# Kernel tuning notes

Hardware: AMD Instinct MI355X
Metric: run time of the kernel (lower is better)

## Reference

```python
import jax, jax.numpy as jnp
import numpy as np

N, E, CLIP, HID, H, P, MD, B = 4096, 16384, 512, 1024, 4, 4, 512, 32
OUT2 = P * MD  # 2048


def prelu(x, a):
    return jnp.where(x >= 0, x, a * x)


def add_self_loops(src, dst, edge_attr, n):
    # PyG fill_value='mean': self-loop edge_attr = mean of incoming edge attrs
    sums = jax.ops.segment_sum(edge_attr, dst, num_segments=n)
    cnt = jax.ops.segment_sum(jnp.ones((dst.shape[0], 1), edge_attr.dtype), dst, num_segments=n)
    loop_attr = sums / jnp.maximum(cnt, 1.0)
    idx = jnp.arange(n)
    return (jnp.concatenate([src, idx]), jnp.concatenate([dst, idx]),
            jnp.concatenate([edge_attr, loop_attr], axis=0))


def gat_conv(x, src, dst, edge_attr, W, asrc, adst, We, ae, bias, heads, c):
    # PyG GATConv, concat=False (mean over heads), edge_dim used only in attention
    n = x.shape[0]
    src, dst, edge_attr = add_self_loops(src, dst, edge_attr, n)
    h = (x @ W).reshape(n, heads, c)                      # [N,H,C]
    e = (edge_attr @ We).reshape(-1, heads, c)            # [E',H,C]
    a_s = jnp.einsum('nhc,hc->nh', h, asrc)
    a_d = jnp.einsum('nhc,hc->nh', h, adst)
    a_e = jnp.einsum('ehc,hc->eh', e, ae)
    alpha = jax.nn.leaky_relu(a_s[src] + a_d[dst] + a_e, 0.2)  # [E',H]
    amax = jax.ops.segment_max(alpha, dst, num_segments=n)
    ex = jnp.exp(alpha - amax[dst])
    denom = jax.ops.segment_sum(ex, dst, num_segments=n)
    w = ex / jnp.maximum(denom[dst], 1e-16)
    msg = h[src] * w[:, :, None]                          # [E',H,C]
    out = jax.ops.segment_sum(msg, dst, num_segments=n)   # [N,H,C]
    return out.mean(axis=1) + bias


def attentional_pool(x, batch, gW1, gb1, gp1, gW2, gb2, gp2, gW3, gb3, n_graphs):
    gate = prelu(x @ gW1 + gb1, gp1)
    gate = prelu(gate @ gW2 + gb2, gp2)
    gate = gate @ gW3 + gb3                               # [N,1]
    gmax = jax.ops.segment_max(gate, batch, num_segments=n_graphs)
    ex = jnp.exp(gate - gmax[batch])
    denom = jax.ops.segment_sum(ex, batch, num_segments=n_graphs)
    s = ex / jnp.maximum(denom[batch], 1e-16)             # [N,1]
    return jax.ops.segment_sum(s * x, batch, num_segments=n_graphs)  # [B,F]


def setup_inputs() -> dict:
    key = jax.random.key(0)
    ks = jax.random.split(key, 24)
    sc = 0.05
    inp = {
        'x': jax.random.normal(ks[0], (N, CLIP), jnp.float32),
        'edge_index': jax.random.randint(ks[1], (2, E), 0, N),
        'edge_attr': jax.random.normal(ks[2], (E, CLIP), jnp.float32),
        'batch': jnp.sort(jax.random.randint(ks[3], (N,), 0, B)),
        # GATConv 1
        'W1': jax.random.normal(ks[4], (CLIP, H * HID), jnp.float32) * sc,
        'asrc1': jax.random.normal(ks[5], (H, HID), jnp.float32) * sc,
        'adst1': jax.random.normal(ks[6], (H, HID), jnp.float32) * sc,
        'We1': jax.random.normal(ks[7], (CLIP, H * HID), jnp.float32) * sc,
        'ae1': jax.random.normal(ks[8], (H, HID), jnp.float32) * sc,
        'b1': jnp.zeros((HID,), jnp.float32),
        'p1': jnp.float32(0.25),
        # GATConv 2
        'W2': jax.random.normal(ks[9], (HID, H * OUT2), jnp.float32) * sc,
        'asrc2': jax.random.normal(ks[10], (H, OUT2), jnp.float32) * sc,
        'adst2': jax.random.normal(ks[11], (H, OUT2), jnp.float32) * sc,
        'We2': jax.random.normal(ks[12], (CLIP, H * OUT2), jnp.float32) * sc,
        'ae2': jax.random.normal(ks[13], (H, OUT2), jnp.float32) * sc,
        'b2': jnp.zeros((OUT2,), jnp.float32),
        'p2': jnp.float32(0.25),
        # AttentionalAggregation gate_nn
        'gW1': jax.random.normal(ks[14], (OUT2, HID), jnp.float32) * sc,
        'gb1': jnp.zeros((HID,), jnp.float32),
        'gp1': jnp.float32(0.25),
        'gW2': jax.random.normal(ks[15], (HID, HID), jnp.float32) * sc,
        'gb2': jnp.zeros((HID,), jnp.float32),
        'gp2': jnp.float32(0.25),
        'gW3': jax.random.normal(ks[16], (HID, 1), jnp.float32) * sc,
        'gb3': jnp.zeros((1,), jnp.float32),
    }
    return inp


def reference(x, edge_index, edge_attr, batch,
              W1, asrc1, adst1, We1, ae1, b1, p1,
              W2, asrc2, adst2, We2, ae2, b2, p2,
              gW1, gb1, gp1, gW2, gb2, gp2, gW3, gb3):
    src, dst = edge_index[0], edge_index[1]
    h = gat_conv(x, src, dst, edge_attr, W1, asrc1, adst1, We1, ae1, b1, H, HID)
    h = prelu(h, p1)
    h = gat_conv(h, src, dst, edge_attr, W2, asrc2, adst2, We2, ae2, b2, H, OUT2)
    h = prelu(h, p2)
    pooled = attentional_pool(h, batch, gW1, gb1, gp1, gW2, gb2, gp2, gW3, gb3, B)
    return pooled.reshape(-1, P, MD)  # [B, prefix_length, mbart_dim]
```

## Files before the change

### kernel.cpp

```cpp
#include <hip/hip_runtime.h>
#include <hip/hip_bf16.h>
#include <math.h>

#define N_NODES 4096
#define N_EDGES 16384
#define CLIPD   512
#define HID     1024
#define NH      4
#define OUTD    2048
#define NB      32

typedef __bf16 bf16_t;
typedef bf16_t bf16x8 __attribute__((ext_vector_type(8)));
typedef float f32x4 __attribute__((ext_vector_type(4)));

static __device__ __forceinline__ float lrelu(float x) { return x >= 0.f ? x : 0.2f * x; }

static __device__ __forceinline__ unsigned short f2bf(float f) {
  union { float f; unsigned int u; } v; v.f = f;
  unsigned int u = v.u;
  unsigned int r = (u + 0x7FFFu + ((u >> 16) & 1u)) >> 16;
  return (unsigned short)r;
}
static __device__ __forceinline__ float bf2f(unsigned short u) {
  union { unsigned int i; float f; } v; v.i = ((unsigned int)u) << 16; return v.f;
}

#define GLDS(g, l) __builtin_amdgcn_global_load_lds( \
    (const __attribute__((address_space(1))) void*)(g), \
    (__attribute__((address_space(3))) void*)(l), 16, 0, 0)

__global__ __launch_bounds__(256) void cvt_kernel(const float* __restrict__ in,
                                                  unsigned short* __restrict__ out, int n4) {
  int i = blockIdx.x * 256 + threadIdx.x;
  if (i < n4) {
    float4 f = ((const float4*)in)[i];
    ushort4 o;
    o.x = f2bf(f.x); o.y = f2bf(f.y); o.z = f2bf(f.z); o.w = f2bf(f.w);
    ((ushort4*)out)[i] = o;
  }
}

__global__ __launch_bounds__(256) void tcvt_kernel(const float* __restrict__ in,
                                                   unsigned short* __restrict__ out,
                                                   int K, int N) {
  __shared__ float t[32][33];
  const int k0 = blockIdx.y * 32, n0 = blockIdx.x * 32;
  const int tx = threadIdx.x, ty = threadIdx.y;
#pragma unroll
  for (int i = 0; i < 4; ++i) t[ty + 8 * i][tx] = in[(size_t)(k0 + ty + 8 * i) * N + n0 + tx];
  __syncthreads();
#pragma unroll
  for (int i = 0; i < 4; ++i) out[(size_t)(n0 + ty + 8 * i) * K + k0 + tx] = f2bf(t[tx][ty + 8 * i]);
}

template<int C>
__global__ __launch_bounds__(256) void v_kernel(const float* __restrict__ We,
                                                const float* __restrict__ ae,
                                                float* __restrict__ v) {
  const int k = blockIdx.x;
  const int tid = threadIdx.x;
  const float* row = We + (size_t)k * (NH * C);
  float acc[NH] = {0.f, 0.f, 0.f, 0.f};
  for (int c = tid; c < C; c += 256) {
    for (int h = 0; h < NH; ++h) acc[h] += row[h * C + c] * ae[h * C + c];
  }
  for (int h = 0; h < NH; ++h)
    for (int o = 32; o > 0; o >>= 1) acc[h] += __shfl_down(acc[h], o);
  __shared__ float red[4][NH];
  const int wid = tid >> 6, lane = tid & 63;
  if (lane == 0)
    for (int h = 0; h < NH; ++h) red[wid][h] = acc[h];
  __syncthreads();
  if (tid < NH) v[k * NH + tid] = red[0][tid] + red[1][tid] + red[2][tid] + red[3][tid];
}

__global__ void deg_kernel(const int* __restrict__ ei, int* __restrict__ deg) {
  int e = blockIdx.x * 256 + threadIdx.x;
  if (e < N_EDGES) atomicAdd(&deg[ei[N_EDGES + e]], 1);
}

__global__ __launch_bounds__(1024) void scan_kernel(const int* __restrict__ deg, int* __restrict__ offs) {
  __shared__ int s[1024];
  const int t = threadIdx.x;
  int d0 = deg[4 * t], d1 = deg[4 * t + 1], d2 = deg[4 * t + 2], d3 = deg[4 * t + 3];
  s[t] = d0 + d1 + d2 + d3;
  __syncthreads();
  for (int off = 1; off < 1024; off <<= 1) {
    int v = (t >= off) ? s[t - off] : 0;
    __syncthreads();
    s[t] += v;
    __syncthreads();
  }
  int base = (t > 0) ? s[t - 1] : 0;
  offs[4 * t] = base;
  offs[4 * t + 1] = base + d0;
  offs[4 * t + 2] = base + d0 + d1;
  offs[4 * t + 3] = base + d0 + d1 + d2;
  if (t == 1023) offs[4096] = s[1023];
}

__global__ void fill_kernel(const int* __restrict__ ei, const int* __restrict__ offs,
                            int* __restrict__ cursor, int* __restrict__ csr_src,
                            int* __restrict__ csr_eid) {
  int e = blockIdx.x * 256 + threadIdx.x;
  if (e >= N_EDGES) return;
  int dst = ei[N_EDGES + e];
  int pos = offs[dst] + atomicAdd(&cursor[dst], 1);
  csr_src[pos] = ei[e];
  csr_eid[pos] = e;
}

__global__ __launch_bounds__(256) void ae_kernel(const float* __restrict__ ea, const int* __restrict__ ei,
                                                 const float* __restrict__ v1, const float* __restrict__ v2,
                                                 float* __restrict__ ae1, float* __restrict__ ae2,
                                                 float* __restrict__ aesum1, float* __restrict__ aesum2) {
  __shared__ float4 v1s[CLIPD];
  __shared__ float4 v2s[CLIPD];
  const int tid = threadIdx.x;
  v1s[tid] = ((const float4*)v1)[tid];
  v1s[tid + 256] = ((const float4*)v1)[tid + 256];
  v2s[tid] = ((const float4*)v2)[tid];
  v2s[tid + 256] = ((const float4*)v2)[tid + 256];
  __syncthreads();
  const int wid = tid >> 6, lane = tid & 63;
  for (int i = 0; i < 16; ++i) {
    const int e = blockIdx.x * 64 + wid * 16 + i;
    const float* row = ea + (size_t)e * CLIPD;
    float a1[NH] = {0.f, 0.f, 0.f, 0.f}, a2[NH] = {0.f, 0.f, 0.f, 0.f};
    for (int k = lane; k < CLIPD; k += 64) {
      float x = row[k];
      float4 w1 = v1s[k];
      float4 w2 = v2s[k];
      a1[0] += x * w1.x; a1[1] += x * w1.y; a1[2] += x * w1.z; a1[3] += x * w1.w;
      a2[0] += x * w2.x; a2[1] += x * w2.y; a2[2] += x * w2.z; a2[3] += x * w2.w;
    }
    for (int h = 0; h < NH; ++h)
      for (int o = 32; o > 0; o >>= 1) {
        a1[h] += __shfl_down(a1[h], o);
        a2[h] += __shfl_down(a2[h], o);
      }
    if (lane == 0) {
      int dst = ei[N_EDGES + e];
      for (int h = 0; h < NH; ++h) {
        ae1[e * NH + h] = a1[h];
        ae2[e * NH + h] = a2[h];
        atomicAdd(&aesum1[dst * NH + h], a1[h]);
        atomicAdd(&aesum2[dst * NH + h], a2[h]);
      }
    }
  }
}

__global__ void loopdiv_kernel(float* __restrict__ s1, float* __restrict__ s2,
                               const int* __restrict__ deg) {
  int i = blockIdx.x * 256 + threadIdx.x;
  if (i >= N_NODES * NH) return;
  float c = fmaxf((float)deg[i >> 2], 1.0f);
  s1[i] /= c;
  s2[i] /= c;
}

template<int EPI>
__global__ __launch_bounds__(256) void mfma_gemm(const unsigned short* __restrict__ A,
                                                 const unsigned short* __restrict__ Bt,
                                                 unsigned short* __restrict__ C,
                                                 int M, int N, int K,
                                                 const float* __restrict__ bias,
                                                 const float* __restrict__ pa) {
  __shared__ unsigned short As[128 * 32];
  __shared__ unsigned short Bs[128 * 32];
  const int tid = threadIdx.x;
  const int lane = tid & 63;
  const int w = tid >> 6;
  const int wr = w >> 1, wc = w & 1;
  const int brow = blockIdx.y * 128, bcol = blockIdx.x * 128;
  const int r0 = tid >> 2;
  const int koff = (tid & 3) * 8;
  const int fr = lane & 15;
  const int fk = (lane >> 4) * 8;
  f32x4 acc[4][4] = {};
  for (int kt = 0; kt < K; kt += 32) {
    GLDS(A + (size_t)(brow + r0) * K + kt + koff, &As[tid * 8]);
    GLDS(A + (size_t)(brow + 64 + r0) * K + kt + koff, &As[2048 + tid * 8]);
    GLDS(Bt + (size_t)(bcol + r0) * K + kt + koff, &Bs[tid * 8]);
    GLDS(Bt + (size_t)(bcol + 64 + r0) * K + kt + koff, &Bs[2048 + tid * 8]);
    asm volatile("s_waitcnt vmcnt(0)" ::: "memory");
    __syncthreads();
    bf16x8 af[4], bfr[4];
#pragma unroll
    for (int mi = 0; mi < 4; ++mi)
      af[mi] = *(const bf16x8*)&As[(wr * 64 + mi * 16 + fr) * 32 + fk];
#pragma unroll
    for (int ni = 0; ni < 4; ++ni)
      bfr[ni] = *(const bf16x8*)&Bs[(wc * 64 + ni * 16 + fr) * 32 + fk];
#pragma unroll
    for (int mi = 0; mi < 4; ++mi)
#pragma unroll
      for (int ni = 0; ni < 4; ++ni)
        acc[mi][ni] = __builtin_amdgcn_mfma_f32_16x16x32_bf16(af[mi], bfr[ni], acc[mi][ni], 0, 0, 0);
    __syncthreads();
  }
  const float ap = EPI ? *pa : 0.f;
#pragma unroll
  for (int mi = 0; mi < 4; ++mi) {
    const int rb = brow + wr * 64 + mi * 16 + (lane >> 4) * 4;
#pragma unroll
    for (int ni = 0; ni < 4; ++ni) {
      const int col = bcol + wc * 64 + ni * 16 + fr;
      float bv = 0.f;
      if (EPI) bv = bias[col];
#pragma unroll
      for (int r = 0; r < 4; ++r) {
        float v = acc[mi][ni][r];
        if (EPI) { v += bv; v = v >= 0.f ? v : ap * v; }
        C[(size_t)(rb + r) * N + col] = f2bf(v);
      }
    }
  }
}

template<int C>
__global__ __launch_bounds__(256) void nodedot_kernel(const unsigned short* __restrict__ hbuf,
                                                      const float* __restrict__ asrc,
                                                      const float* __restrict__ adst,
                                                      float* __restrict__ as_, float* __restrict__ ad_) {
  const int n = blockIdx.x, tid = threadIdx.x;
  const unsigned short* row = hbuf + (size_t)n * (NH * C);
  float s[NH] = {0.f, 0.f, 0.f, 0.f}, d[NH] = {0.f, 0.f, 0.f, 0.f};
  for (int c4 = tid; c4 < C / 4; c4 += 256) {
#pragma unroll
    for (int h = 0; h < NH; ++h) {
      ushort4 u = *(const ushort4*)&row[h * C + c4 * 4];
      float4 av = *(const float4*)&asrc[h * C + c4 * 4];
      float4 dv = *(const float4*)&adst[h * C + c4 * 4];
      float f0 = bf2f(u.x), f1 = bf2f(u.y), f2 = bf2f(u.z), f3 = bf2f(u.w);
      s[h] += f0 * av.x + f1 * av.y + f2 * av.z + f3 * av.w;
      d[h] += f0 * dv.x + f1 * dv.y + f2 * dv.z + f3 * dv.w;
    }
  }
  for (int h = 0; h < NH; ++h)
    for (int o = 32; o > 0; o >>= 1) {
      s[h] += __shfl_down(s[h], o);
      d[h] += __shfl_down(d[h], o);
    }
  __shared__ float rs[4][NH], rd[4][NH];
  const int wid = tid >> 6, lane = tid & 63;
  if (lane == 0)
    for (int h = 0; h < NH; ++h) {
      rs[wid][h] = s[h];
      rd[wid][h] = d[h];
    }
  __syncthreads();
  if (tid < NH)
    as_[n * NH + tid] = rs[0][tid] + rs[1][tid] + rs[2][tid] + rs[3][tid];
  else if (tid < 2 * NH) {
    int h = tid - NH;
    ad_[n * NH + h] = rd[0][h] + rd[1][h] + rd[2][h] + rd[3][h];
  }
}

template<int C, int OUTMODE>
__global__ __launch_bounds__(256) void agg_kernel(const unsigned short* __restrict__ hbuf,
                                                  const float* __restrict__ as_, const float* __restrict__ ad_,
                                                  const float* __restrict__ aee, const float* __restrict__ aeloop,
                                                  const int* __restrict__ offs, const int* __restrict__ csr_src,
                                                  const int* __restrict__ csr_eid,
                                                  const float* __restrict__ bias, const float* __restrict__ pa,
                                                  float* __restrict__ outf, unsigned short* __restrict__ outb) {
  constexpr int HC = NH * C;
  constexpr int C4 = C / 1024;
  const int n = blockIdx.x;
  const int tid = threadIdx.x;
  const int off = offs[n];
  const int deg = offs[n + 1] - off;
  __shared__ float minv[NH], dinv[NH], wself[NH];
  __shared__ float wch[32][NH];
  __shared__ int sch[32];
  if (tid < 64) {
    const int h = tid >> 4, slot = tid & 15;
    const float adn = ad_[n * NH + h];
    const float aself = lrelu(as_[n * NH + h] + adn + aeloop[n * NH + h]);
    float m = (slot == 0) ? aself : -3.0e38f;
    for (int i = slot; i < deg; i += 16) {
      float a = lrelu(as_[csr_src[off + i] * NH + h] + adn + aee[csr_eid[off + i] * NH + h]);
      m = fmaxf(m, a);
    }
    for (int o = 1; o < 16; o <<= 1) m = fmaxf(m, __shfl_xor(m, o));
    float den = (slot == 0) ? __expf(aself - m) : 0.f;
    for (int i = slot; i < deg; i += 16) {
      float a = lrelu(as_[csr_src[off + i] * NH + h] + adn + aee[csr_eid[off + i] * NH + h]);
      den += __expf(a - m);
    }
    for (int o = 1; o < 16; o <<= 1) den += __shfl_xor(den, o);
    if (slot == 0) {
      minv[h] = m;
      dinv[h] = 1.0f / den;
      wself[h] = __expf(aself - m) / den;
    }
  }
  __syncthreads();
  float acc[NH][C4 * 4];
#pragma unroll
  for (int h = 0; h < NH; ++h)
#pragma unroll
    for (int c = 0; c < C4 * 4; ++c) acc[h][c] = 0.f;
  for (int base = 0; base < deg; base += 32) {
    const int cnt = min(32, deg - base);
    if (tid < cnt * NH) {
      const int i = tid >> 2, h = tid & 3;
      const int sidx = csr_src[off + base + i];
      float a = lrelu(as_[sidx * NH + h] + ad_[n * NH + h] + aee[csr_eid[off + base + i] * NH + h]);
      wch[i][h] = __expf(a - minv[h]) * dinv[h];
      if (h == 0) sch[i] = sidx;
    }
    __syncthreads();
    for (int i = 0; i < cnt; ++i) {
      const unsigned short* hp = hbuf + (size_t)sch[i] * HC;
#pragma unroll
      for (int h = 0; h < NH; ++h) {
        const float wv = wch[i][h];
#pragma unroll
        for (int c = 0; c < C4; ++c) {
          ushort4 u = *(const ushort4*)&hp[h * C + (c * 256 + tid) * 4];
          acc[h][c * 4 + 0] += wv * bf2f(u.x);
          acc[h][c * 4 + 1] += wv * bf2f(u.y);
          acc[h][c * 4 + 2] += wv * bf2f(u.z);
          acc[h][c * 4 + 3] += wv * bf2f(u.w);
        }
      }
    }
    __syncthreads();
  }
  {
    const unsigned short* hp = hbuf + (size_t)n * HC;
#pragma unroll
    for (int h = 0; h < NH; ++h) {
      const float wv = wself[h];
#pragma unroll
      for (int c = 0; c < C4; ++c) {
        ushort4 u = *(const ushort4*)&hp[h * C + (c * 256 + tid) * 4];
        acc[h][c * 4 + 0] += wv * bf2f(u.x);
        acc[h][c * 4 + 1] += wv * bf2f(u.y);
        acc[h][c * 4 + 2] += wv * bf2f(u.z);
        acc[h][c * 4 + 3] += wv * bf2f(u.w);
      }
    }
  }
  const float ap = *pa;
#pragma unroll
  for (int c = 0; c < C4; ++c) {
    const int cb = (c * 256 + tid) * 4;
    float4 vf;
    ushort4 vb;
    float* vp = &vf.x;
#pragma unroll
    for (int j = 0; j < 4; ++j) {
      float v = 0.25f * (acc[0][c * 4 + j] + acc[1][c * 4 + j] + acc[2][c * 4 + j] + acc[3][c * 4 + j])
                + bias[cb + j];
      v = v >= 0.f ? v : ap * v;
      vp[j] = v;
    }
    vb.x = f2bf(vf.x); vb.y = f2bf(vf.y); vb.z = f2bf(vf.z); vb.w = f2bf(vf.w);
    if (OUTMODE == 1) *(float4*)&outf[(size_t)n * C + cb] = vf;
    *(ushort4*)&outb[(size_t)n * C + cb] = vb;
  }
}

__global__ __launch_bounds__(256) void gate3_kernel(const unsigned short* __restrict__ gh2,
                                                    const float* __restrict__ gW3,
                                                    const float* __restrict__ gb3, float* __restrict__ gate) {
  const int n = blockIdx.x, tid = threadIdx.x;
  const unsigned short* row = gh2 + (size_t)n * HID;
  ushort4 u = *(const ushort4*)&row[tid * 4];
  float4 wv = *(const float4*)&gW3[tid * 4];
  float acc = bf2f(u.x) * wv.x + bf2f(u.y) * wv.y + bf2f(u.z) * wv.z + bf2f(u.w) * wv.w;
  for (int o = 32; o > 0; o >>= 1) acc += __shfl_down(acc, o);
  __shared__ float red[4];
  const int wid = tid >> 6, lane = tid & 63;
  if (lane == 0) red[wid] = acc;
  __syncthreads();
  if (tid == 0) gate[n] = red[0] + red[1] + red[2] + red[3] + gb3[0];
}

__global__ void gstart_kernel(const int* __restrict__ batch, int* __restrict__ gstart) {
  int n = blockIdx.x * 256 + threadIdx.x;
  if (n >= N_NODES) return;
  int b = batch[n];
  if (n == 0) {
    for (int bb = 0; bb <= b; ++bb) gstart[bb] = 0;
  } else {
    int pb = batch[n - 1];
    for (int bb = pb + 1; bb <= b; ++bb) gstart[bb] = n;
  }
  if (n == N_NODES - 1)
    for (int bb = b + 1; bb <= NB; ++bb) gstart[bb] = N_NODES;
}

__global__ __launch_bounds__(256) void gsoft_kernel(const float* __restrict__ gate, const int* __restrict__ gstart,
                                                    float* __restrict__ gm, float* __restrict__ ginv) {
  const int b = blockIdx.x, tid = threadIdx.x;
  const int s = gstart[b], e = gstart[b + 1];
  float m = -3.0e38f;
  for (int n = s + tid; n < e; n += 256) m = fmaxf(m, gate[n]);
  for (int o = 32; o > 0; o >>= 1) m = fmaxf(m, __shfl_down(m, o));
  __shared__ float red[4];
  __shared__ float red2[4];
  const int wid = tid >> 6, lane = tid & 63;
  if (lane == 0) red[wid] = m;
  __syncthreads();
  m = fmaxf(fmaxf(red[0], red[1]), fmaxf(red[2], red[3]));
  float sum = 0.f;
  for (int n = s + tid; n < e; n += 256) sum += __expf(gate[n] - m);
  for (int o = 32; o > 0; o >>= 1) sum += __shfl_down(sum, o);
  if (lane == 0) red2[wid] = sum;
  __syncthreads();
  if (tid == 0) {
    sum = red2[0] + red2[1] + red2[2] + red2[3];
    gm[b] = m;
    ginv[b] = 1.0f / fmaxf(sum, 1e-16f);
  }
}

__global__ __launch_bounds__(256) void pool_kernel(const float* __restrict__ out2, const float* __restrict__ gate,
                                                   const float* __restrict__ gm, const float* __restrict__ ginv,
                                                   const int* __restrict__ gstart, float* __restrict__ dout) {
  const int b = blockIdx.y;
  const int col = blockIdx.x * 256 + threadIdx.x;
  const int s = gstart[b], e = gstart[b + 1];
  const float m = gm[b], gi = ginv[b];
  float acc = 0.f;
  for (int n = s; n < e; ++n) {
    float w = __expf(gate[n] - m) * gi;
    acc += w * out2[(size_t)n * OUTD + col];
  }
  dout[(size_t)b * OUTD + col] = acc;
}

#define MB(x) ((size_t)(x) * 1048576)
#define WS_XB     MB(0)
#define WS_W1T    MB(4)
#define WS_H1B    MB(8)
#define WS_H2B    MB(0)
#define WS_OUT1B  MB(64)
#define WS_W2T    MB(72)
#define WS_OUT2F  MB(88)
#define WS_OUT2B  MB(120)
#define WS_GH1B   MB(136)
#define WS_GH2B   MB(144)
#define WS_GW1T   MB(152)
#define WS_GW2T   MB(156)
#define WS_SM     MB(158)
#define WS_DEG    (WS_SM + 0)
#define WS_CUR    (WS_SM + 16384)
#define WS_AES1   (WS_SM + 32768)
#define WS_AES2   (WS_SM + 98304)
#define WS_ZBYTES 163840
#define WS_OFFS   (WS_SM + 163840)
#define WS_CSRS   (WS_OFFS + 16640)
#define WS_CSRE   (WS_CSRS + 65536)
#define WS_AS1    (WS_CSRE + 65536)
#define WS_AD1    (WS_AS1 + 65536)
#define WS_AEE1   (WS_AD1 + 65536)
#define WS_AS2    (WS_AEE1 + 262144)
#define WS_AD2    (WS_AS2 + 65536)
#define WS_AEE2   (WS_AD2 + 65536)
#define WS_V1     (WS_AEE2 + 262144)
#define WS_V2     (WS_V1 + 8192)
#define WS_GATE   (WS_V2 + 8192)
#define WS_GM     (WS_GATE + 16384)
#define WS_GINV   (WS_GM + 128)
#define WS_GSTART (WS_GINV + 128)

extern "C" void kernel_launch(void* const* d_in, const int* in_sizes, int n_in,
                              void* d_out, int out_size, void* d_ws, size_t ws_size,
                              hipStream_t stream) {
  const float* x     = (const float*)d_in[0];
  const int*   ei    = (const int*)d_in[1];
  const float* ea    = (const float*)d_in[2];
  const int*   batch = (const int*)d_in[3];
  const float* W1    = (const float*)d_in[4];
  const float* asrc1 = (const float*)d_in[5];
  const float* adst1 = (const float*)d_in[6];
  const float* We1   = (const float*)d_in[7];
  const float* ae1w  = (const float*)d_in[8];
  const float* b1    = (const float*)d_in[9];
  const float* p1    = (const float*)d_in[10];
  const float* W2    = (const float*)d_in[11];
  const float* asrc2 = (const float*)d_in[12];
  const float* adst2 = (const float*)d_in[13];
  const float* We2   = (const float*)d_in[14];
  const float* ae2w  = (const float*)d_in[15];
  const float* b2    = (const float*)d_in[16];
  const float* p2    = (const float*)d_in[17];
  const float* gW1   = (const float*)d_in[18];
  const float* gb1   = (const float*)d_in[19];
  const float* gp1   = (const float*)d_in[20];
  const float* gW2   = (const float*)d_in[21];
  const float* gb2   = (const float*)d_in[22];
  const float* gp2   = (const float*)d_in[23];
  const float* gW3   = (const float*)d_in[24];
  const float* gb3   = (const float*)d_in[25];

  char* ws = (char*)d_ws;
  unsigned short* xb    = (unsigned short*)(ws + WS_XB);
  unsigned short* W1t   = (unsigned short*)(ws + WS_W1T);
  unsigned short* h1b   = (unsigned short*)(ws + WS_H1B);
  unsigned short* h2b   = (unsigned short*)(ws + WS_H2B);
  unsigned short* out1b = (unsigned short*)(ws + WS_OUT1B);
  unsigned short* W2t   = (unsigned short*)(ws + WS_W2T);
  float*          out2f = (float*)(ws + WS_OUT2F);
  unsigned short* out2b = (unsigned short*)(ws + WS_OUT2B);
  unsigned short* gh1b  = (unsigned short*)(ws + WS_GH1B);
  unsigned short* gh2b  = (unsigned short*)(ws + WS_GH2B);
  unsigned short* gW1t  = (unsigned short*)(ws + WS_GW1T);
  unsigned short* gW2t  = (unsigned short*)(ws + WS_GW2T);
  int*   deg     = (int*)(ws + WS_DEG);
  int*   cursor  = (int*)(ws + WS_CUR);
  float* aesum1  = (float*)(ws + WS_AES1);
  float* aesum2  = (float*)(ws + WS_AES2);
  int*   offs    = (int*)(ws + WS_OFFS);
  int*   csr_src = (int*)(ws + WS_CSRS);
  int*   csr_eid = (int*)(ws + WS_CSRE);
  float* as1     = (float*)(ws + WS_AS1);
  float* ad1     = (float*)(ws + WS_AD1);
  float* aee1    = (float*)(ws + WS_AEE1);
  float* as2     = (float*)(ws + WS_AS2);
  float* ad2     = (float*)(ws + WS_AD2);
  float* aee2    = (float*)(ws + WS_AEE2);
  float* v1      = (float*)(ws + WS_V1);
  float* v2      = (float*)(ws + WS_V2);
  float* gate    = (float*)(ws + WS_GATE);
  float* gm      = (float*)(ws + WS_GM);
  float* ginv    = (float*)(ws + WS_GINV);
  int*   gstart  = (int*)(ws + WS_GSTART);
  float* dout    = (float*)d_out;

  hipMemsetAsync(ws + WS_DEG, 0, WS_ZBYTES, stream);

  cvt_kernel<<<(N_NODES * CLIPD / 4 + 255) / 256, 256, 0, stream>>>(x, xb, N_NODES * CLIPD / 4);
  tcvt_kernel<<<dim3(4096 / 32, 512 / 32), dim3(32, 8), 0, stream>>>(W1, W1t, CLIPD, NH * HID);
  tcvt_kernel<<<dim3(8192 / 32, 1024 / 32), dim3(32, 8), 0, stream>>>(W2, W2t, HID, NH * OUTD);
  tcvt_kernel<<<dim3(1024 / 32, 2048 / 32), dim3(32, 8), 0, stream>>>(gW1, gW1t, OUTD, HID);
  tcvt_kernel<<<dim3(1024 / 32, 1024 / 32), dim3(32, 8), 0, stream>>>(gW2, gW2t, HID, HID);

  v_kernel<HID><<<CLIPD, 256, 0, stream>>>(We1, ae1w, v1);
  v_kernel<OUTD><<<CLIPD, 256, 0, stream>>>(We2, ae2w, v2);

  deg_kernel<<<N_EDGES / 256, 256, 0, stream>>>(ei, deg);
  scan_kernel<<<1, 1024, 0, stream>>>(deg, offs);
  fill_kernel<<<N_EDGES / 256, 256, 0, stream>>>(ei, offs, cursor, csr_src, csr_eid);

  mfma_gemm<0><<<dim3(32, 32), 256, 0, stream>>>(xb, W1t, h1b, N_NODES, NH * HID, CLIPD, nullptr, nullptr);

  ae_kernel<<<N_EDGES / 64, 256, 0, stream>>>(ea, ei, v1, v2, aee1, aee2, aesum1, aesum2);
  loopdiv_kernel<<<(N_NODES * NH) / 256, 256, 0, stream>>>(aesum1, aesum2, deg);

  nodedot_kernel<HID><<<N_NODES, 256, 0, stream>>>(h1b, asrc1, adst1, as1, ad1);
  agg_kernel<HID, 0><<<N_NODES, 256, 0, stream>>>(h1b, as1, ad1, aee1, aesum1, offs, csr_src, csr_eid,
                                                  b1, p1, nullptr, out1b);

  mfma_gemm<0><<<dim3(64, 32), 256, 0, stream>>>(out1b, W2t, h2b, N_NODES, NH * OUTD, HID, nullptr, nullptr);

  nodedot_kernel<OUTD><<<N_NODES, 256, 0, stream>>>(h2b, asrc2, adst2, as2, ad2);
  agg_kernel<OUTD, 1><<<N_NODES, 256, 0, stream>>>(h2b, as2, ad2, aee2, aesum2, offs, csr_src, csr_eid,
                                                   b2, p2, out2f, out2b);

  mfma_gemm<1><<<dim3(8, 32), 256, 0, stream>>>(out2b, gW1t, gh1b, N_NODES, HID, OUTD, gb1, gp1);
  mfma_gemm<1><<<dim3(8, 32), 256, 0, stream>>>(gh1b, gW2t, gh2b, N_NODES, HID, HID, gb2, gp2);
  gate3_kernel<<<N_NODES, 256, 0, stream>>>(gh2b, gW3, gb3, gate);

  gstart_kernel<<<N_NODES / 256, 256, 0, stream>>>(batch, gstart);
  gsoft_kernel<<<NB, 256, 0, stream>>>(gate, gstart, gm, ginv);
  pool_kernel<<<dim3(OUTD / 256, NB), 256, 0, stream>>>(out2f, gate, gm, ginv, gstart, dout);
}
```

Before: 585.9 us.

## Aggregate before projecting in GAT layers and fold attention vectors into weights

Each GAT layer now aggregates per-head attention-weighted input features (x or out1) first. It then does a single GEMM against per-head stacked transposed weights, scaled by 0.25 so the head mean folds into K, with the bias and PReLU applied in the GEMM epilogue. The attention logits a_s and a_d are computed directly from the input rows using precomputed W·asrc and W·adst vectors, which removes the need to materialize the wide h = xW tensor. This shrinks the gather traffic from NH*C-wide rows to input-width rows and removes the large [N, H*C] intermediates. In exchange the GEMM K dimension grows by NH, and attention is now computed on fp32 x or bf16 out1 rather than on the bf16 projected features.

```diff
diff --git a/kernel.cpp b/kernel.cpp
--- a/kernel.cpp
+++ b/kernel.cpp
@@ -54,16 +54,33 @@
   for (int i = 0; i < 4; ++i) out[(size_t)(n0 + ty + 8 * i) * K + k0 + tx] = f2bf(t[tx][ty + 8 * i]);
 }
 
+template<int K1, int N1>
+__global__ __launch_bounds__(256) void stack_tcvt_kernel(const float* __restrict__ in,
+                                                         unsigned short* __restrict__ out,
+                                                         float scale) {
+  __shared__ float t[32][33];
+  const int h = blockIdx.z;
+  const int k0 = blockIdx.y * 32, n0 = blockIdx.x * 32;
+  const int tx = threadIdx.x, ty = threadIdx.y;
+#pragma unroll
+  for (int i = 0; i < 4; ++i)
+    t[ty + 8 * i][tx] = in[(size_t)(k0 + ty + 8 * i) * (NH * N1) + h * N1 + n0 + tx];
+  __syncthreads();
+#pragma unroll
+  for (int i = 0; i < 4; ++i)
+    out[(size_t)(n0 + ty + 8 * i) * (NH * K1) + h * K1 + k0 + tx] = f2bf(scale * t[tx][ty + 8 * i]);
+}
+
 template<int C>
-__global__ __launch_bounds__(256) void v_kernel(const float* __restrict__ We,
-                                                const float* __restrict__ ae,
+__global__ __launch_bounds__(256) void v_kernel(const float* __restrict__ W,
+                                                const float* __restrict__ a,
                                                 float* __restrict__ v) {
   const int k = blockIdx.x;
   const int tid = threadIdx.x;
-  const float* row = We + (size_t)k * (NH * C);
+  const float* row = W + (size_t)k * (NH * C);
   float acc[NH] = {0.f, 0.f, 0.f, 0.f};
   for (int c = tid; c < C; c += 256) {
-    for (int h = 0; h < NH; ++h) acc[h] += row[h * C + c] * ae[h * C + c];
+    for (int h = 0; h < NH; ++h) acc[h] += row[h * C + c] * a[h * C + c];
   }
   for (int h = 0; h < NH; ++h)
     for (int o = 32; o > 0; o >>= 1) acc[h] += __shfl_down(acc[h], o);
@@ -73,6 +90,39 @@
     for (int h = 0; h < NH; ++h) red[wid][h] = acc[h];
   __syncthreads();
   if (tid < NH) v[k * NH + tid] = red[0][tid] + red[1][tid] + red[2][tid] + red[3][tid];
+}
+
+template<int C>
+__global__ __launch_bounds__(256) void v2_kernel(const float* __restrict__ W,
+                                                 const float* __restrict__ a1v,
+                                                 const float* __restrict__ a2v,
+                                                 float* __restrict__ o1, float* __restrict__ o2) {
+  const int k = blockIdx.x;
+  const int tid = threadIdx.x;
+  const float* row = W + (size_t)k * (NH * C);
+  float x1[NH] = {0.f, 0.f, 0.f, 0.f}, x2[NH] = {0.f, 0.f, 0.f, 0.f};
+  for (int c = tid; c < C; c += 256) {
+    for (int h = 0; h < NH; ++h) {
+      float w = row[h * C + c];
+      x1[h] += w * a1v[h * C + c];
+      x2[h] += w * a2v[h * C + c];
+    }
+  }
+  for (int h = 0; h < NH; ++h)
+    for (int o = 32; o > 0; o >>= 1) {
+      x1[h] += __shfl_down(x1[h], o);
+      x2[h] += __shfl_down(x2[h], o);
+    }
+  __shared__ float r1[4][NH], r2[4][NH];
+  const int wid = tid >> 6, lane = tid & 63;
+  if (lane == 0)
+    for (int h = 0; h < NH; ++h) { r1[wid][h] = x1[h]; r2[wid][h] = x2[h]; }
+  __syncthreads();
+  if (tid < NH) o1[k * NH + tid] = r1[0][tid] + r1[1][tid] + r1[2][tid] + r1[3][tid];
+  else if (tid < 2 * NH) {
+    int h = tid - NH;
+    o2[k * NH + h] = r2[0][h] + r2[1][h] + r2[2][h] + r2[3][h];
+  }
 }
 
 __global__ void deg_kernel(const int* __restrict__ ei, int* __restrict__ deg) {
@@ -161,10 +211,184 @@
   s2[i] /= c;
 }
 
-template<int EPI>
+__global__ __launch_bounds__(256) void rowdot_x(const float* __restrict__ x,
+                                                const float* __restrict__ us, const float* __restrict__ ud,
+                                                float* __restrict__ as_, float* __restrict__ ad_) {
+  __shared__ float4 su[CLIPD], sd[CLIPD];
+  const int tid = threadIdx.x;
+  for (int k = tid; k < CLIPD; k += 256) {
+    su[k] = ((const float4*)us)[k];
+    sd[k] = ((const float4*)ud)[k];
+  }
+  __syncthreads();
+  const int wid = tid >> 6, lane = tid & 63;
+  const int n = blockIdx.x * 4 + wid;
+  const float* row = x + (size_t)n * CLIPD;
+  float s[NH] = {0.f, 0.f, 0.f, 0.f}, d[NH] = {0.f, 0.f, 0.f, 0.f};
+  for (int k = lane; k < CLIPD; k += 64) {
+    float xv = row[k];
+    float4 u = su[k], v = sd[k];
+    s[0] += xv * u.x; s[1] += xv * u.y; s[2] += xv * u.z; s[3] += xv * u.w;
+    d[0] += xv * v.x; d[1] += xv * v.y; d[2] += xv * v.z; d[3] += xv * v.w;
+  }
+#pragma unroll
+  for (int h = 0; h < NH; ++h)
+    for (int o = 32; o > 0; o >>= 1) {
+      s[h] += __shfl_down(s[h], o);
+      d[h] += __shfl_down(d[h], o);
+    }
+  if (lane == 0)
+    for (int h = 0; h < NH; ++h) {
+      as_[n * NH + h] = s[h];
+      ad_[n * NH + h] = d[h];
+    }
+}
+
+__global__ __launch_bounds__(256) void rowdot_o(const unsigned short* __restrict__ rows,
+                                                const float* __restrict__ us, const float* __restrict__ ud,
+                                                float* __restrict__ as_, float* __restrict__ ad_) {
+  __shared__ float4 su[HID], sd[HID];
+  const int tid = threadIdx.x;
+  for (int k = tid; k < HID; k += 256) {
+    su[k] = ((const float4*)us)[k];
+    sd[k] = ((const float4*)ud)[k];
+  }
+  __syncthreads();
+  const int wid = tid >> 6, lane = tid & 63;
+  const int n = blockIdx.x * 4 + wid;
+  const unsigned short* row = rows + (size_t)n * HID;
+  float s[NH] = {0.f, 0.f, 0.f, 0.f}, d[NH] = {0.f, 0.f, 0.f, 0.f};
+  for (int k2 = lane; k2 < HID / 2; k2 += 64) {
+    ushort2 uv = ((const ushort2*)row)[k2];
+    float f0 = bf2f(uv.x), f1 = bf2f(uv.y);
+    float4 u0 = su[2 * k2], u1 = su[2 * k2 + 1];
+    float4 v0 = sd[2 * k2], v1 = sd[2 * k2 + 1];
+    s[0] += f0 * u0.x + f1 * u1.x; s[1] += f0 * u0.y + f1 * u1.y;
+    s[2] += f0 * u0.z + f1 * u1.z; s[3] += f0 * u0.w + f1 * u1.w;
+    d[0] += f0 * v0.x + f1 * v1.x; d[1] += f0 * v0.y + f1 * v1.y;
+    d[2] += f0 * v0.z + f1 * v1.z; d[3] += f0 * v0.w + f1 * v1.w;
+  }
+#pragma unroll
+  for (int h = 0; h < NH; ++h)
+    for (int o = 32; o > 0; o >>= 1) {
+      s[h] += __shfl_down(s[h], o);
+      d[h] += __shfl_down(d[h], o);
+    }
+  if (lane == 0)
+    for (int h = 0; h < NH; ++h) {
+      as_[n * NH + h] = s[h];
+      ad_[n * NH + h] = d[h];
+    }
+}
+
+template<int C>
+__global__ __launch_bounds__(256) void aggn_kernel(const unsigned short* __restrict__ src,
+                                                   const float* __restrict__ as_, const float* __restrict__ ad_,
+                                                   const float* __restrict__ aee, const float* __restrict__ aeloop,
+                                                   const int* __restrict__ offs, const int* __restrict__ csr_src,
+                                                   const int* __restrict__ csr_eid,
+                                                   unsigned short* __restrict__ out) {
+  constexpr int CPT = C / 256;
+  const int n = blockIdx.x;
+  const int tid = threadIdx.x;
+  const int off = offs[n];
+  const int deg = offs[n + 1] - off;
+  __shared__ float minv[NH], dinv[NH], wself[NH];
+  __shared__ float wch[32][NH];
+  __shared__ int sch[32];
+  if (tid < 64) {
+    const int h = tid >> 4, slot = tid & 15;
+    const float adn = ad_[n * NH + h];
+    const float aself = lrelu(as_[n * NH + h] + adn + aeloop[n * NH + h]);
+    float m = (slot == 0) ? aself : -3.0e38f;
+    for (int i = slot; i < deg; i += 16) {
+      float a = lrelu(as_[csr_src[off + i] * NH + h] + adn + aee[csr_eid[off + i] * NH + h]);
+      m = fmaxf(m, a);
+    }
+    for (int o = 1; o < 16; o <<= 1) m = fmaxf(m, __shfl_xor(m, o));
+    float den = (slot == 0) ? __expf(aself - m) : 0.f;
+    for (int i = slot; i < deg; i += 16) {
+      float a = lrelu(as_[csr_src[off + i] * NH + h] + adn + aee[csr_eid[off + i] * NH + h]);
+      den += __expf(a - m);
+    }
+    for (int o = 1; o < 16; o <<= 1) den += __shfl_xor(den, o);
+    if (slot == 0) {
+      minv[h] = m;
+      dinv[h] = 1.0f / den;
+      wself[h] = __expf(aself - m) / den;
+    }
+  }
+  __syncthreads();
+  float acc[NH][CPT];
+#pragma unroll
+  for (int h = 0; h < NH; ++h)
+#pragma unroll
+    for (int c = 0; c < CPT; ++c) acc[h][c] = 0.f;
+  for (int base = 0; base < deg; base += 32) {
+    const int cnt = min(32, deg - base);
+    if (tid < cnt * NH) {
+      const int i = tid >> 2, h = tid & 3;
+      const int sidx = csr_src[off + base + i];
+      float a = lrelu(as_[sidx * NH + h] + ad_[n * NH + h] + aee[csr_eid[off + base + i] * NH + h]);
+      wch[i][h] = __expf(a - minv[h]) * dinv[h];
+      if (h == 0) sch[i] = sidx;
+    }
+    __syncthreads();
+    for (int i = 0; i < cnt; ++i) {
+      const unsigned short* hp = src + (size_t)sch[i] * C + tid * CPT;
+      float f[CPT];
+      if constexpr (CPT == 2) {
+        ushort2 u = *(const ushort2*)hp;
+        f[0] = bf2f(u.x); f[1] = bf2f(u.y);
+      } else {
+        ushort4 u = *(const ushort4*)hp;
+        f[0] = bf2f(u.x); f[1] = bf2f(u.y); f[2] = bf2f(u.z); f[3] = bf2f(u.w);
+      }
+#pragma unroll
+      for (int h = 0; h < NH; ++h) {
+        const float wv = wch[i][h];
+#pragma unroll
+        for (int c = 0; c < CPT; ++c) acc[h][c] += wv * f[c];
+      }
+    }
+    __syncthreads();
+  }
+  {
+    const unsigned short* hp = src + (size_t)n * C + tid * CPT;
+    float f[CPT];
+    if constexpr (CPT == 2) {
+      ushort2 u = *(const ushort2*)hp;
+      f[0] = bf2f(u.x); f[1] = bf2f(u.y);
+    } else {
+      ushort4 u = *(const ushort4*)hp;
+      f[0] = bf2f(u.x); f[1] = bf2f(u.y); f[2] = bf2f(u.z); f[3] = bf2f(u.w);
+    }
+#pragma unroll
+    for (int h = 0; h < NH; ++h) {
+      const float wv = wself[h];
+#pragma unroll
+      for (int c = 0; c < CPT; ++c) acc[h][c] += wv * f[c];
+    }
+  }
+#pragma unroll
+  for (int h = 0; h < NH; ++h) {
+    if constexpr (CPT == 2) {
+      ushort2 o;
+      o.x = f2bf(acc[h][0]); o.y = f2bf(acc[h][1]);
+      *(ushort2*)&out[((size_t)n * NH + h) * C + tid * 2] = o;
+    } else {
+      ushort4 o;
+      o.x = f2bf(acc[h][0]); o.y = f2bf(acc[h][1]); o.z = f2bf(acc[h][2]); o.w = f2bf(acc[h][3]);
+      *(ushort4*)&out[((size_t)n * NH + h) * C + tid * 4] = o;
+    }
+  }
+}
+
+template<int EPI, int WF>
 __global__ __launch_bounds__(256) void mfma_gemm(const unsigned short* __restrict__ A,
                                                  const unsigned short* __restrict__ Bt,
                                                  unsigned short* __restrict__ C,
+                                                 float* __restrict__ Cf,
                                                  int M, int N, int K,
                                                  const float* __restrict__ bias,
                                                  const float* __restrict__ pa) {
@@ -215,155 +439,9 @@
         float v = acc[mi][ni][r];
         if (EPI) { v += bv; v = v >= 0.f ? v : ap * v; }
         C[(size_t)(rb + r) * N + col] = f2bf(v);
+        if (WF) Cf[(size_t)(rb + r) * N + col] = v;
       }
     }
-  }
-}
-
-template<int C>
-__global__ __launch_bounds__(256) void nodedot_kernel(const unsigned short* __restrict__ hbuf,
-                                                      const float* __restrict__ asrc,
-                                                      const float* __restrict__ adst,
-                                                      float* __restrict__ as_, float* __restrict__ ad_) {
-  const int n = blockIdx.x, tid = threadIdx.x;
-  const unsigned short* row = hbuf + (size_t)n * (NH * C);
-  float s[NH] = {0.f, 0.f, 0.f, 0.f}, d[NH] = {0.f, 0.f, 0.f, 0.f};
-  for (int c4 = tid; c4 < C / 4; c4 += 256) {
-#pragma unroll
-    for (int h = 0; h < NH; ++h) {
-      ushort4 u = *(const ushort4*)&row[h * C + c4 * 4];
-      float4 av = *(const float4*)&asrc[h * C + c4 * 4];
-      float4 dv = *(const float4*)&adst[h * C + c4 * 4];
-      float f0 = bf2f(u.x), f1 = bf2f(u.y), f2 = bf2f(u.z), f3 = bf2f(u.w);
-      s[h] += f0 * av.x + f1 * av.y + f2 * av.z + f3 * av.w;
-      d[h] += f0 * dv.x + f1 * dv.y + f2 * dv.z + f3 * dv.w;
-    }
-  }
-  for (int h = 0; h < NH; ++h)
-    for (int o = 32; o > 0; o >>= 1) {
-      s[h] += __shfl_down(s[h], o);
-      d[h] += __shfl_down(d[h], o);
-    }
-  __shared__ float rs[4][NH], rd[4][NH];
-  const int wid = tid >> 6, lane = tid & 63;
-  if (lane == 0)
-    for (int h = 0; h < NH; ++h) {
-      rs[wid][h] = s[h];
-      rd[wid][h] = d[h];
-    }
-  __syncthreads();
-  if (tid < NH)
-    as_[n * NH + tid] = rs[0][tid] + rs[1][tid] + rs[2][tid] + rs[3][tid];
-  else if (tid < 2 * NH) {
-    int h = tid - NH;
-    ad_[n * NH + h] = rd[0][h] + rd[1][h] + rd[2][h] + rd[3][h];
-  }
-}
-
-template<int C, int OUTMODE>
-__global__ __launch_bounds__(256) void agg_kernel(const unsigned short* __restrict__ hbuf,
-                                                  const float* __restrict__ as_, const float* __restrict__ ad_,
-                                                  const float* __restrict__ aee, const float* __restrict__ aeloop,
-                                                  const int* __restrict__ offs, const int* __restrict__ csr_src,
-                                                  const int* __restrict__ csr_eid,
-                                                  const float* __restrict__ bias, const float* __restrict__ pa,
-                                                  float* __restrict__ outf, unsigned short* __restrict__ outb) {
-  constexpr int HC = NH * C;
-  constexpr int C4 = C / 1024;
-  const int n = blockIdx.x;
-  const int tid = threadIdx.x;
-  const int off = offs[n];
-  const int deg = offs[n + 1] - off;
-  __shared__ float minv[NH], dinv[NH], wself[NH];
-  __shared__ float wch[32][NH];
-  __shared__ int sch[32];
-  if (tid < 64) {
-    const int h = tid >> 4, slot = tid & 15;
-    const float adn = ad_[n * NH + h];
-    const float aself = lrelu(as_[n * NH + h] + adn + aeloop[n * NH + h]);
-    float m = (slot == 0) ? aself : -3.0e38f;
-    for (int i = slot; i < deg; i += 16) {
-      float a = lrelu(as_[csr_src[off + i] * NH + h] + adn + aee[csr_eid[off + i] * NH + h]);
-      m = fmaxf(m, a);
-    }
-    for (int o = 1; o < 16; o <<= 1) m = fmaxf(m, __shfl_xor(m, o));
-    float den = (slot == 0) ? __expf(aself - m) : 0.f;
-    for (int i = slot; i < deg; i += 16) {
-      float a = lrelu(as_[csr_src[off + i] * NH + h] + adn + aee[csr_eid[off + i] * NH + h]);
-      den += __expf(a - m);
-    }
-    for (int o = 1; o < 16; o <<= 1) den += __shfl_xor(den, o);
-    if (slot == 0) {
-      minv[h] = m;
-      dinv[h] = 1.0f / den;
-      wself[h] = __expf(aself - m) / den;
-    }
-  }
-  __syncthreads();
-  float acc[NH][C4 * 4];
-#pragma unroll
-  for (int h = 0; h < NH; ++h)
-#pragma unroll
-    for (int c = 0; c < C4 * 4; ++c) acc[h][c] = 0.f;
-  for (int base = 0; base < deg; base += 32) {
-    const int cnt = min(32, deg - base);
-    if (tid < cnt * NH) {
-      const int i = tid >> 2, h = tid & 3;
-      const int sidx = csr_src[off + base + i];
-      float a = lrelu(as_[sidx * NH + h] + ad_[n * NH + h] + aee[csr_eid[off + base + i] * NH + h]);
-      wch[i][h] = __expf(a - minv[h]) * dinv[h];
-      if (h == 0) sch[i] = sidx;
-    }
-    __syncthreads();
-    for (int i = 0; i < cnt; ++i) {
-      const unsigned short* hp = hbuf + (size_t)sch[i] * HC;
-#pragma unroll
-      for (int h = 0; h < NH; ++h) {
-        const float wv = wch[i][h];
-#pragma unroll
-        for (int c = 0; c < C4; ++c) {
-          ushort4 u = *(const ushort4*)&hp[h * C + (c * 256 + tid) * 4];
-          acc[h][c * 4 + 0] += wv * bf2f(u.x);
-          acc[h][c * 4 + 1] += wv * bf2f(u.y);
-          acc[h][c * 4 + 2] += wv * bf2f(u.z);
-          acc[h][c * 4 + 3] += wv * bf2f(u.w);
-        }
-      }
-    }
-    __syncthreads();
-  }
-  {
-    const unsigned short* hp = hbuf + (size_t)n * HC;
-#pragma unroll
-    for (int h = 0; h < NH; ++h) {
-      const float wv = wself[h];
-#pragma unroll
-      for (int c = 0; c < C4; ++c) {
-        ushort4 u = *(const ushort4*)&hp[h * C + (c * 256 + tid) * 4];
-        acc[h][c * 4 + 0] += wv * bf2f(u.x);
-        acc[h][c * 4 + 1] += wv * bf2f(u.y);
-        acc[h][c * 4 + 2] += wv * bf2f(u.z);
-        acc[h][c * 4 + 3] += wv * bf2f(u.w);
-      }
-    }
-  }
-  const float ap = *pa;
-#pragma unroll
-  for (int c = 0; c < C4; ++c) {
-    const int cb = (c * 256 + tid) * 4;
-    float4 vf;
-    ushort4 vb;
-    float* vp = &vf.x;
-#pragma unroll
-    for (int j = 0; j < 4; ++j) {
-      float v = 0.25f * (acc[0][c * 4 + j] + acc[1][c * 4 + j] + acc[2][c * 4 + j] + acc[3][c * 4 + j])
-                + bias[cb + j];
-      v = v >= 0.f ? v : ap * v;
-      vp[j] = v;
-    }
-    vb.x = f2bf(vf.x); vb.y = f2bf(vf.y); vb.z = f2bf(vf.z); vb.w = f2bf(vf.w);
-    if (OUTMODE == 1) *(float4*)&outf[(size_t)n * C + cb] = vf;
-    *(ushort4*)&outb[(size_t)n * C + cb] = vb;
   }
 }
 
@@ -439,18 +517,18 @@
 
 #define MB(x) ((size_t)(x) * 1048576)
 #define WS_XB     MB(0)
-#define WS_W1T    MB(4)
-#define WS_H1B    MB(8)
-#define WS_H2B    MB(0)
-#define WS_OUT1B  MB(64)
-#define WS_W2T    MB(72)
-#define WS_OUT2F  MB(88)
-#define WS_OUT2B  MB(120)
-#define WS_GH1B   MB(136)
-#define WS_GH2B   MB(144)
-#define WS_GW1T   MB(152)
-#define WS_GW2T   MB(156)
-#define WS_SM     MB(158)
+#define WS_B1T    MB(4)
+#define WS_B2T    MB(8)
+#define WS_GW1T   MB(24)
+#define WS_GW2T   MB(28)
+#define WS_AGGX   MB(30)
+#define WS_OUT1B  MB(46)
+#define WS_AGGO   MB(54)
+#define WS_OUT2F  MB(86)
+#define WS_OUT2B  MB(118)
+#define WS_GH1B   MB(134)
+#define WS_GH2B   MB(142)
+#define WS_SM     MB(150)
 #define WS_DEG    (WS_SM + 0)
 #define WS_CUR    (WS_SM + 16384)
 #define WS_AES1   (WS_SM + 32768)
@@ -467,7 +545,11 @@
 #define WS_AEE2   (WS_AD2 + 65536)
 #define WS_V1     (WS_AEE2 + 262144)
 #define WS_V2     (WS_V1 + 8192)
-#define WS_GATE   (WS_V2 + 8192)
+#define WS_US1    (WS_V2 + 8192)
+#define WS_UD1    (WS_US1 + 8192)
+#define WS_US2    (WS_UD1 + 8192)
+#define WS_UD2    (WS_US2 + 16384)
+#define WS_GATE   (WS_UD2 + 16384)
 #define WS_GM     (WS_GATE + 16384)
 #define WS_GINV   (WS_GM + 128)
 #define WS_GSTART (WS_GINV + 128)
@@ -504,17 +586,17 @@
 
   char* ws = (char*)d_ws;
   unsigned short* xb    = (unsigned short*)(ws + WS_XB);
-  unsigned short* W1t   = (unsigned short*)(ws + WS_W1T);
-  unsigned short* h1b   = (unsigned short*)(ws + WS_H1B);
-  unsigned short* h2b   = (unsigned short*)(ws + WS_H2B);
+  unsigned short* B1t   = (unsigned short*)(ws + WS_B1T);
+  unsigned short* B2t   = (unsigned short*)(ws + WS_B2T);
+  unsigned short* gW1t  = (unsigned short*)(ws + WS_GW1T);
+  unsigned short* gW2t  = (unsigned short*)(ws + WS_GW2T);
+  unsigned short* aggXb = (unsigned short*)(ws + WS_AGGX);
   unsigned short* out1b = (unsigned short*)(ws + WS_OUT1B);
-  unsigned short* W2t   = (unsigned short*)(ws + WS_W2T);
+  unsigned short* aggOb = (unsigned short*)(ws + WS_AGGO);
   float*          out2f = (float*)(ws + WS_OUT2F);
   unsigned short* out2b = (unsigned short*)(ws + WS_OUT2B);
   unsigned short* gh1b  = (unsigned short*)(ws + WS_GH1B);
   unsigned short* gh2b  = (unsigned short*)(ws + WS_GH2B);
-  unsigned short* gW1t  = (unsigned short*)(ws + WS_GW1T);
-  unsigned short* gW2t  = (unsigned short*)(ws + WS_GW2T);
   int*   deg     = (int*)(ws + WS_DEG);
   int*   cursor  = (int*)(ws + WS_CUR);
   float* aesum1  = (float*)(ws + WS_AES1);
@@ -530,6 +612,10 @@
   float* aee2    = (float*)(ws + WS_AEE2);
   float* v1      = (float*)(ws + WS_V1);
   float* v2      = (float*)(ws + WS_V2);
+  float* us1     = (float*)(ws + WS_US1);
+  float* ud1     = (float*)(ws + WS_UD1);
+  float* us2     = (float*)(ws + WS_US2);
+  float* ud2     = (float*)(ws + WS_UD2);
   float* gate    = (float*)(ws + WS_GATE);
   float* gm      = (float*)(ws + WS_GM);
   float* ginv    = (float*)(ws + WS_GINV);
@@ -539,35 +625,37 @@
   hipMemsetAsync(ws + WS_DEG, 0, WS_ZBYTES, stream);
 
   cvt_kernel<<<(N_NODES * CLIPD / 4 + 255) / 256, 256, 0, stream>>>(x, xb, N_NODES * CLIPD / 4);
-  tcvt_kernel<<<dim3(4096 / 32, 512 / 32), dim3(32, 8), 0, stream>>>(W1, W1t, CLIPD, NH * HID);
-  tcvt_kernel<<<dim3(8192 / 32, 1024 / 32), dim3(32, 8), 0, stream>>>(W2, W2t, HID, NH * OUTD);
-  tcvt_kernel<<<dim3(1024 / 32, 2048 / 32), dim3(32, 8), 0, stream>>>(gW1, gW1t, OUTD, HID);
-  tcvt_kernel<<<dim3(1024 / 32, 1024 / 32), dim3(32, 8), 0, stream>>>(gW2, gW2t, HID, HID);
+  stack_tcvt_kernel<CLIPD, HID><<<dim3(HID / 32, CLIPD / 32, NH), dim3(32, 8), 0, stream>>>(W1, B1t, 0.25f);
+  stack_tcvt_kernel<HID, OUTD><<<dim3(OUTD / 32, HID / 32, NH), dim3(32, 8), 0, stream>>>(W2, B2t, 0.25f);
+  tcvt_kernel<<<dim3(HID / 32, OUTD / 32), dim3(32, 8), 0, stream>>>(gW1, gW1t, OUTD, HID);
+  tcvt_kernel<<<dim3(HID / 32, HID / 32), dim3(32, 8), 0, stream>>>(gW2, gW2t, HID, HID);
 
   v_kernel<HID><<<CLIPD, 256, 0, stream>>>(We1, ae1w, v1);
   v_kernel<OUTD><<<CLIPD, 256, 0, stream>>>(We2, ae2w, v2);
+  v2_kernel<HID><<<CLIPD, 256, 0, stream>>>(W1, asrc1, adst1, us1, ud1);
+  v2_kernel<OUTD><<<HID, 256, 0, stream>>>(W2, asrc2, adst2, us2, ud2);
 
   deg_kernel<<<N_EDGES / 256, 256, 0, stream>>>(ei, deg);
   scan_kernel<<<1, 1024, 0, stream>>>(deg, offs);
   fill_kernel<<<N_EDGES / 256, 256, 0, stream>>>(ei, offs, cursor, csr_src, csr_eid);
 
-  mfma_gemm<0><<<dim3(32, 32), 256, 0, stream>>>(xb, W1t, h1b, N_NODES, NH * HID, CLIPD, nullptr, nullptr);
-
   ae_kernel<<<N_EDGES / 64, 256, 0, stream>>>(ea, ei, v1, v2, aee1, aee2, aesum1, aesum2);
   loopdiv_kernel<<<(N_NODES * NH) / 256, 256, 0, stream>>>(aesum1, aesum2, deg);
 
-  nodedot_kernel<HID><<<N_NODES, 256, 0, stream>>>(h1b, asrc1, adst1, as1, ad1);
-  agg_kernel<HID, 0><<<N_NODES, 256, 0, stream>>>(h1b, as1, ad1, aee1, aesum1, offs, csr_src, csr_eid,
-                                                  b1, p1, nullptr, out1b);
-
-  mfma_gemm<0><<<dim3(64, 32), 256, 0, stream>>>(out1b, W2t, h2b, N_NODES, NH * OUTD, HID, nullptr, nullptr);
-
-  nodedot_kernel<OUTD><<<N_NODES, 256, 0, stream>>>(h2b, asrc2, adst2, as2, ad2);
-  agg_kernel<OUTD, 1><<<N_NODES, 256, 0, stream>>>(h2b, as2, ad2, aee2, aesum2, offs, csr_src, csr_eid,
-                                                   b2, p2, out2f, out2b);
-
-  mfma_gemm<1><<<dim3(8, 32), 256, 0, stream>>>(out2b, gW1t, gh1b, N_NODES, HID, OUTD, gb1, gp1);
-  mfma_gemm<1><<<dim3(8, 32), 256, 0, stream>>>(gh1b, gW2t, gh2b, N_NODES, HID, HID, gb2, gp2);
+  rowdot_x<<<N_NODES / 4, 256, 0, stream>>>(x, us1, ud1, as1, ad1);
+  aggn_kernel<CLIPD><<<N_NODES, 256, 0, stream>>>(xb, as1, ad1, aee1, aesum1, offs, csr_src, csr_eid, aggXb);
+  mfma_gemm<1, 0><<<dim3(HID / 128, N_NODES / 128), 256, 0, stream>>>(
+      aggXb, B1t, out1b, nullptr, N_NODES, HID, NH * CLIPD, b1, p1);
+
+  rowdot_o<<<N_NODES / 4, 256, 0, stream>>>(out1b, us2, ud2, as2, ad2);
+  aggn_kernel<HID><<<N_NODES, 256, 0, stream>>>(out1b, as2, ad2, aee2, aesum2, offs, csr_src, csr_eid, aggOb);
+  mfma_gemm<1, 1><<<dim3(OUTD / 128, N_NODES / 128), 256, 0, stream>>>(
+      aggOb, B2t, out2b, out2f, N_NODES, OUTD, NH * HID, b2, p2);
+
+  mfma_gemm<1, 0><<<dim3(HID / 128, N_NODES / 128), 256, 0, stream>>>(
+      out2b, gW1t, gh1b, nullptr, N_NODES, HID, OUTD, gb1, gp1);
+  mfma_gemm<1, 0><<<dim3(HID / 128, N_NODES / 128), 256, 0, stream>>>(
+      gh1b, gW2t, gh2b, nullptr, N_NODES, HID, HID, gb2, gp2);
   gate3_kernel<<<N_NODES, 256, 0, stream>>>(gh2b, gW3, gb3, gate);
 
   gstart_kernel<<<N_NODES / 256, 256, 0, stream>>>(batch, gstart);
```

Measured after the change: 559.0 us. 4.6% less time.
